# Kernel optimization log

Hardware: AMD Instinct MI355X
Metric: run time of the kernel (lower is better)

The kernel has to match this reference:

```python
import math
import jax, jax.numpy as jnp
import numpy as np
from jax import lax

# Block_mamba(dim=192): x = x + Mamba(LN1(x)); x = x + EinFFT(LN2(x), H, W)
DIM = 192
D_STATE = 64
D_CONV = 4
EXPAND = 2
D_INNER = EXPAND * DIM          # 384
DT_RANK = math.ceil(DIM / 16)   # 12
NUM_BLOCKS = 4                  # EinFFT hardcoded
BLOCK_SIZE = DIM // NUM_BLOCKS  # 48
LAMBDA = 0.01                   # softshrink threshold


def setup_inputs() -> dict:
    key = jax.random.key(0)
    ks = jax.random.split(key, 20)
    B, N, C = 4, 1024, DIM
    s = 0.02
    x = jax.random.normal(ks[0], (B, N, C), jnp.float32)
    inp = {
        "x": x,
        "ln1_w": jnp.ones((C,), jnp.float32),
        "ln1_b": jnp.zeros((C,), jnp.float32),
        "in_proj_w": jax.random.normal(ks[1], (2 * D_INNER, C), jnp.float32) * s,
        "conv_w": jax.random.normal(ks[2], (D_INNER, 1, D_CONV), jnp.float32) * 0.1,
        "conv_b": jnp.zeros((D_INNER,), jnp.float32),
        "x_proj_w": jax.random.normal(ks[3], (DT_RANK + 2 * D_STATE, D_INNER), jnp.float32) * s,
        "dt_proj_w": jax.random.normal(ks[4], (D_INNER, DT_RANK), jnp.float32) * (DT_RANK ** -0.5),
        "dt_proj_b": jax.random.uniform(ks[5], (D_INNER,), jnp.float32, -4.0, -2.0),
        "A_log": jnp.log(jnp.broadcast_to(jnp.arange(1, D_STATE + 1, dtype=jnp.float32), (D_INNER, D_STATE))),
        "D": jnp.ones((D_INNER,), jnp.float32),
        "out_proj_w": jax.random.normal(ks[6], (C, D_INNER), jnp.float32) * s,
        "ln2_w": jnp.ones((C,), jnp.float32),
        "ln2_b": jnp.zeros((C,), jnp.float32),
        "cw1": jax.random.normal(ks[7], (2, NUM_BLOCKS, BLOCK_SIZE, BLOCK_SIZE), jnp.float32) * s,
        "cw2": jax.random.normal(ks[8], (2, NUM_BLOCKS, BLOCK_SIZE, BLOCK_SIZE), jnp.float32) * s,
        "cb1": jax.random.normal(ks[9], (2, NUM_BLOCKS, BLOCK_SIZE), jnp.float32) * s,
        "cb2": jax.random.normal(ks[10], (2, NUM_BLOCKS, BLOCK_SIZE), jnp.float32) * s,
        "H": 32,
        "W": 32,
    }
    return inp


def layer_norm(x, w, b, eps=1e-5):
    mu = jnp.mean(x, axis=-1, keepdims=True)
    var = jnp.var(x, axis=-1, keepdims=True)
    return (x - mu) * lax.rsqrt(var + eps) * w + b


def mamba(x, in_proj_w, conv_w, conv_b, x_proj_w, dt_proj_w, dt_proj_b, A_log, D):
    B, L, C = x.shape
    xz = jnp.einsum('blc,ec->ble', x, in_proj_w)          # [B,L,2*D_INNER]
    xm, z = jnp.split(xz, 2, axis=-1)                      # each [B,L,D_INNER]
    # causal depthwise conv1d (torch pads both sides then slices [:, :, :L])
    xc = lax.conv_general_dilated(
        xm.transpose(0, 2, 1), conv_w, (1,), [(D_CONV - 1, 0)],
        dimension_numbers=('NCH', 'OIH', 'NCH'), feature_group_count=D_INNER)
    xm = jax.nn.silu(xc + conv_b[None, :, None]).transpose(0, 2, 1)  # [B,L,D_INNER]
    dbc = jnp.einsum('bld,ed->ble', xm, x_proj_w)
    dt, Bm, Cm = jnp.split(dbc, [DT_RANK, DT_RANK + D_STATE], axis=-1)
    delta = jax.nn.softplus(jnp.einsum('blr,dr->bld', dt, dt_proj_w) + dt_proj_b)  # [B,L,D_INNER]
    A = -jnp.exp(A_log)                                    # [D_INNER, D_STATE]

    def step(h, inp):
        d_t, B_t, C_t, x_t = inp                           # [B,d],[B,n],[B,n],[B,d]
        dA = jnp.exp(d_t[:, :, None] * A)                  # [B,d,n]
        h = h * dA + (d_t * x_t)[:, :, None] * B_t[:, None, :]
        y = jnp.einsum('bdn,bn->bd', h, C_t)
        return h, y

    h0 = jnp.zeros((B, D_INNER, D_STATE), x.dtype)
    xs = (delta.transpose(1, 0, 2), Bm.transpose(1, 0, 2), Cm.transpose(1, 0, 2), xm.transpose(1, 0, 2))
    _, ys = lax.scan(step, h0, xs)                         # ys: [L,B,d]
    y = ys.transpose(1, 0, 2) + xm * D
    y = y * jax.nn.silu(z)
    return jnp.einsum('bld,cd->blc', y, out_proj_w_global[0])


# small trick to keep mamba signature tidy
out_proj_w_global = [None]


def einfft(x, cw1, cw2, cb1, cb2):
    B, N, C = x.shape
    xv = x.reshape(B, N, NUM_BLOCKS, BLOCK_SIZE)
    pad1 = (1 << math.ceil(math.log2(N))) - N
    pad2 = (1 << math.ceil(math.log2(NUM_BLOCKS))) - NUM_BLOCKS
    if pad1 or pad2:
        xv = jnp.pad(xv, ((0, 0), (0, pad1), (0, pad2), (0, 0)))
    X = jnp.fft.fft2(xv, axes=(1, 2), norm='ortho')
    mul = lambda t, w: jnp.einsum('Bnbd,bdk->Bnbk', t, w)
    r1 = jax.nn.relu(mul(X.real, cw1[0]) - mul(X.imag, cw1[1]) + cb1[0])
    i1 = jax.nn.relu(mul(X.real, cw1[1]) + mul(X.imag, cw1[0]) + cb1[1])
    r2 = mul(r1, cw2[0]) - mul(i1, cw2[1]) + cb2[0]
    i2 = mul(r1, cw2[1]) + mul(i1, cw2[0]) + cb2[1]
    ss = lambda v: jnp.where(v > LAMBDA, v - LAMBDA, jnp.where(v < -LAMBDA, v + LAMBDA, jnp.zeros((), v.dtype)))
    Z = ss(r2) + 1j * ss(i2)
    y = jnp.fft.ifft2(Z, axes=(1, 2), norm='ortho')[:, :N, :NUM_BLOCKS, :]
    return y.real.reshape(B, N, C)  # torch .to(real dtype) keeps real part


def reference(x, ln1_w, ln1_b, in_proj_w, conv_w, conv_b, x_proj_w, dt_proj_w, dt_proj_b,
              A_log, D, out_proj_w, ln2_w, ln2_b, cw1, cw2, cb1, cb2, H, W):
    out_proj_w_global[0] = out_proj_w
    x = x + mamba(layer_norm(x, ln1_w, ln1_b), in_proj_w, conv_w, conv_b,
                  x_proj_w, dt_proj_w, dt_proj_b, A_log, D)
    x = x + einfft(layer_norm(x, ln2_w, ln2_b), cw1, cw2, cb1, cb2)
    return x
```

## Files before the change

kernel.cpp:

```cpp
#include <hip/hip_runtime.h>
#include <math.h>

#define PI_F 3.14159265358979323846f

__device__ __forceinline__ float lane_bcast(float v, int l) {
  return __int_as_float(__builtin_amdgcn_readlane(__float_as_int(v), l));
}

__device__ __forceinline__ float wave_reduce_sum(float v) {
  v += __shfl_xor(v, 32, 64);
  v += __shfl_xor(v, 16, 64);
  v += __shfl_xor(v, 8, 64);
  v += __shfl_xor(v, 4, 64);
  v += __shfl_xor(v, 2, 64);
  v += __shfl_xor(v, 1, 64);
  return v;
}

__global__ __launch_bounds__(256) void ln_kernel(const float* __restrict__ x,
    const float* __restrict__ w, const float* __restrict__ b, float* __restrict__ o) {
  int row = blockIdx.x * 4 + (threadIdx.x >> 6);
  int lane = threadIdx.x & 63;
  const float* xr = x + (size_t)row * 192;
  float v0 = xr[lane], v1 = xr[lane + 64], v2 = xr[lane + 128];
  float s  = wave_reduce_sum(v0 + v1 + v2);
  float s2 = wave_reduce_sum(v0 * v0 + v1 * v1 + v2 * v2);
  float mu  = s * (1.f / 192.f);
  float var = s2 * (1.f / 192.f) - mu * mu;
  float rs  = rsqrtf(var + 1e-5f);
  float* orow = o + (size_t)row * 192;
  orow[lane]       = (v0 - mu) * rs * w[lane]       + b[lane];
  orow[lane + 64]  = (v1 - mu) * rs * w[lane + 64]  + b[lane + 64];
  orow[lane + 128] = (v2 - mu) * rs * w[lane + 128] + b[lane + 128];
}

__global__ __launch_bounds__(256) void ln2t_kernel(const float* __restrict__ x,
    const float* __restrict__ w, const float* __restrict__ b, float* __restrict__ xT) {
  __shared__ float xt[32][193];
  __shared__ float mu_s[32], rs_s[32];
  int blk = blockIdx.x;
  int Bi = blk >> 5;
  int t0 = (blk & 31) * 32;
  int tid = threadIdx.x;
  const float* xb = x + ((size_t)(Bi * 1024 + t0)) * 192;
  for (int i = tid; i < 32 * 192; i += 256) {
    xt[i / 192][i % 192] = xb[i];
  }
  __syncthreads();
  int row = tid >> 3, seg = tid & 7;
  float s = 0.f, s2 = 0.f;
  const float* xr = &xt[row][seg * 24];
#pragma unroll
  for (int k = 0; k < 24; ++k) { float v = xr[k]; s += v; s2 += v * v; }
  s  += __shfl_xor(s, 1, 64);  s  += __shfl_xor(s, 2, 64);  s  += __shfl_xor(s, 4, 64);
  s2 += __shfl_xor(s2, 1, 64); s2 += __shfl_xor(s2, 2, 64); s2 += __shfl_xor(s2, 4, 64);
  if (seg == 0) {
    float mu = s * (1.f / 192.f);
    float var = s2 * (1.f / 192.f) - mu * mu;
    mu_s[row] = mu;
    rs_s[row] = rsqrtf(var + 1e-5f);
  }
  __syncthreads();
  for (int i = tid; i < 32 * 192; i += 256) {
    int ch = i >> 5, r2 = i & 31;
    float v = (xt[r2][ch] - mu_s[r2]) * rs_s[r2] * w[ch] + b[ch];
    xT[((size_t)(Bi * 192 + ch)) * 1024 + t0 + r2] = v;
  }
}

__global__ __launch_bounds__(256) void gemm_tn(const float* __restrict__ A,
    const float* __restrict__ W, const float* __restrict__ res, float* __restrict__ C,
    int M, int N, int K) {
  __shared__ float As[2][32][68];
  __shared__ float Ws[2][32][68];
  int tid = threadIdx.x;
  int m0 = blockIdx.y * 64, n0 = blockIdx.x * 64;
  int tr = tid >> 4, tc = tid & 15;
  int sm  = tid >> 3;
  int skq = tid & 7;
  float4 aP[2], wP[2];
#pragma unroll
  for (int j = 0; j < 2; ++j) {
    int m = sm + j * 32;
    aP[j] = *(const float4*)(A + (size_t)(m0 + m) * K + skq * 4);
    int n = n0 + m;
    if (n < N) wP[j] = *(const float4*)(W + (size_t)n * K + skq * 4);
    else       wP[j] = make_float4(0.f, 0.f, 0.f, 0.f);
  }
#pragma unroll
  for (int j = 0; j < 2; ++j) {
    int m = sm + j * 32;
    As[0][skq * 4 + 0][m] = aP[j].x;
    As[0][skq * 4 + 1][m] = aP[j].y;
    As[0][skq * 4 + 2][m] = aP[j].z;
    As[0][skq * 4 + 3][m] = aP[j].w;
    Ws[0][skq * 4 + 0][m] = wP[j].x;
    Ws[0][skq * 4 + 1][m] = wP[j].y;
    Ws[0][skq * 4 + 2][m] = wP[j].z;
    Ws[0][skq * 4 + 3][m] = wP[j].w;
  }
  __syncthreads();
  float acc[4][4] = {{0.f}};
  int nk = K >> 5;
  for (int it = 0; it < nk; ++it) {
    int cur = it & 1, nxt = cur ^ 1;
    if (it + 1 < nk) {
      int kk = (it + 1) << 5;
#pragma unroll
      for (int j = 0; j < 2; ++j) {
        int m = sm + j * 32;
        aP[j] = *(const float4*)(A + (size_t)(m0 + m) * K + kk + skq * 4);
        int n = n0 + m;
        if (n < N) wP[j] = *(const float4*)(W + (size_t)n * K + kk + skq * 4);
        else       wP[j] = make_float4(0.f, 0.f, 0.f, 0.f);
      }
    }
#pragma unroll
    for (int k = 0; k < 32; ++k) {
      float4 a4 = *(const float4*)&As[cur][k][tr * 4];
      float4 w4 = *(const float4*)&Ws[cur][k][tc * 4];
      float a[4] = {a4.x, a4.y, a4.z, a4.w};
      float bb[4] = {w4.x, w4.y, w4.z, w4.w};
#pragma unroll
      for (int i = 0; i < 4; ++i)
#pragma unroll
        for (int j = 0; j < 4; ++j)
          acc[i][j] = fmaf(a[i], bb[j], acc[i][j]);
    }
    if (it + 1 < nk) {
#pragma unroll
      for (int j = 0; j < 2; ++j) {
        int m = sm + j * 32;
        As[nxt][skq * 4 + 0][m] = aP[j].x;
        As[nxt][skq * 4 + 1][m] = aP[j].y;
        As[nxt][skq * 4 + 2][m] = aP[j].z;
        As[nxt][skq * 4 + 3][m] = aP[j].w;
        Ws[nxt][skq * 4 + 0][m] = wP[j].x;
        Ws[nxt][skq * 4 + 1][m] = wP[j].y;
        Ws[nxt][skq * 4 + 2][m] = wP[j].z;
        Ws[nxt][skq * 4 + 3][m] = wP[j].w;
      }
      __syncthreads();
    }
  }
#pragma unroll
  for (int i = 0; i < 4; ++i) {
    int m = m0 + tr * 4 + i;
#pragma unroll
    for (int j = 0; j < 4; ++j) {
      int n = n0 + tc * 4 + j;
      if (n < N) {
        float v = acc[i][j];
        if (res) v += res[m * N + n];
        C[m * N + n] = v;
      }
    }
  }
}

__global__ __launch_bounds__(256) void gemm_tn32(const float* __restrict__ A,
    const float* __restrict__ W, const float* __restrict__ res, float* __restrict__ C,
    int M, int N, int K) {
  __shared__ float As[2][32][36];
  __shared__ float Ws[2][32][68];
  int tid = threadIdx.x;
  int m0 = blockIdx.y * 32, n0 = blockIdx.x * 64;
  int tr = tid >> 4, tc = tid & 15;
  int sm  = tid >> 3;
  int skq = tid & 7;
  float4 aP, wP[2];
  aP = *(const float4*)(A + (size_t)(m0 + sm) * K + skq * 4);
#pragma unroll
  for (int j = 0; j < 2; ++j) {
    int n = n0 + sm + j * 32;
    if (n < N) wP[j] = *(const float4*)(W + (size_t)n * K + skq * 4);
    else       wP[j] = make_float4(0.f, 0.f, 0.f, 0.f);
  }
  As[0][skq * 4 + 0][sm] = aP.x;
  As[0][skq * 4 + 1][sm] = aP.y;
  As[0][skq * 4 + 2][sm] = aP.z;
  As[0][skq * 4 + 3][sm] = aP.w;
#pragma unroll
  for (int j = 0; j < 2; ++j) {
    int n = sm + j * 32;
    Ws[0][skq * 4 + 0][n] = wP[j].x;
    Ws[0][skq * 4 + 1][n] = wP[j].y;
    Ws[0][skq * 4 + 2][n] = wP[j].z;
    Ws[0][skq * 4 + 3][n] = wP[j].w;
  }
  __syncthreads();
  float acc[2][4] = {{0.f}};
  int nk = K >> 5;
  for (int it = 0; it < nk; ++it) {
    int cur = it & 1, nxt = cur ^ 1;
    if (it + 1 < nk) {
      int kk = (it + 1) << 5;
      aP = *(const float4*)(A + (size_t)(m0 + sm) * K + kk + skq * 4);
#pragma unroll
      for (int j = 0; j < 2; ++j) {
        int n = n0 + sm + j * 32;
        if (n < N) wP[j] = *(const float4*)(W + (size_t)n * K + kk + skq * 4);
        else       wP[j] = make_float4(0.f, 0.f, 0.f, 0.f);
      }
    }
#pragma unroll
    for (int k = 0; k < 32; ++k) {
      float2 a2 = *(const float2*)&As[cur][k][tr * 2];
      float4 w4 = *(const float4*)&Ws[cur][k][tc * 4];
      float a[2] = {a2.x, a2.y};
      float bb[4] = {w4.x, w4.y, w4.z, w4.w};
#pragma unroll
      for (int i = 0; i < 2; ++i)
#pragma unroll
        for (int j = 0; j < 4; ++j)
          acc[i][j] = fmaf(a[i], bb[j], acc[i][j]);
    }
    if (it + 1 < nk) {
      As[nxt][skq * 4 + 0][sm] = aP.x;
      As[nxt][skq * 4 + 1][sm] = aP.y;
      As[nxt][skq * 4 + 2][sm] = aP.z;
      As[nxt][skq * 4 + 3][sm] = aP.w;
#pragma unroll
      for (int j = 0; j < 2; ++j) {
        int n = sm + j * 32;
        Ws[nxt][skq * 4 + 0][n] = wP[j].x;
        Ws[nxt][skq * 4 + 1][n] = wP[j].y;
        Ws[nxt][skq * 4 + 2][n] = wP[j].z;
        Ws[nxt][skq * 4 + 3][n] = wP[j].w;
      }
      __syncthreads();
    }
  }
#pragma unroll
  for (int i = 0; i < 2; ++i) {
    int m = m0 + tr * 2 + i;
#pragma unroll
    for (int j = 0; j < 4; ++j) {
      int n = n0 + tc * 4 + j;
      if (n < N) {
        float v = acc[i][j];
        if (res) v += res[m * N + n];
        C[m * N + n] = v;
      }
    }
  }
}

__global__ __launch_bounds__(256) void gemm_at32(const float* __restrict__ AT,
    const float* __restrict__ W, const float* __restrict__ res, float* __restrict__ C,
    int M, int N, int K) {
  __shared__ float As[2][32][36];
  __shared__ float Ws[2][32][68];
  int tid = threadIdx.x;
  int m0 = blockIdx.y * 32, n0 = blockIdx.x * 64;
  int bb = m0 >> 10;
  int t0 = m0 & 1023;
  const float* Ab = AT + ((size_t)bb * K) * 1024 + t0;
  int tr = tid >> 4, tc = tid & 15;
  int sm  = tid >> 3;
  int skq = tid & 7;
  float4 aP, wP[2];
  aP = *(const float4*)(Ab + (size_t)sm * 1024 + skq * 4);
#pragma unroll
  for (int j = 0; j < 2; ++j) {
    int n = n0 + sm + j * 32;
    if (n < N) wP[j] = *(const float4*)(W + (size_t)n * K + skq * 4);
    else       wP[j] = make_float4(0.f, 0.f, 0.f, 0.f);
  }
  *(float4*)&As[0][sm][skq * 4] = aP;
#pragma unroll
  for (int j = 0; j < 2; ++j) {
    int n = sm + j * 32;
    Ws[0][skq * 4 + 0][n] = wP[j].x;
    Ws[0][skq * 4 + 1][n] = wP[j].y;
    Ws[0][skq * 4 + 2][n] = wP[j].z;
    Ws[0][skq * 4 + 3][n] = wP[j].w;
  }
  __syncthreads();
  float acc[2][4] = {{0.f}};
  int nk = K >> 5;
  for (int it = 0; it < nk; ++it) {
    int cur = it & 1, nxt = cur ^ 1;
    if (it + 1 < nk) {
      int kk = (it + 1) << 5;
      aP = *(const float4*)(Ab + (size_t)(kk + sm) * 1024 + skq * 4);
#pragma unroll
      for (int j = 0; j < 2; ++j) {
        int n = n0 + sm + j * 32;
        if (n < N) wP[j] = *(const float4*)(W + (size_t)n * K + kk + skq * 4);
        else       wP[j] = make_float4(0.f, 0.f, 0.f, 0.f);
      }
    }
#pragma unroll
    for (int k = 0; k < 32; ++k) {
      float2 a2 = *(const float2*)&As[cur][k][tr * 2];
      float4 w4 = *(const float4*)&Ws[cur][k][tc * 4];
      float a[2] = {a2.x, a2.y};
      float bb4[4] = {w4.x, w4.y, w4.z, w4.w};
#pragma unroll
      for (int i = 0; i < 2; ++i)
#pragma unroll
        for (int j = 0; j < 4; ++j)
          acc[i][j] = fmaf(a[i], bb4[j], acc[i][j]);
    }
    if (it + 1 < nk) {
      *(float4*)&As[nxt][sm][skq * 4] = aP;
#pragma unroll
      for (int j = 0; j < 2; ++j) {
        int n = sm + j * 32;
        Ws[nxt][skq * 4 + 0][n] = wP[j].x;
        Ws[nxt][skq * 4 + 1][n] = wP[j].y;
        Ws[nxt][skq * 4 + 2][n] = wP[j].z;
        Ws[nxt][skq * 4 + 3][n] = wP[j].w;
      }
      __syncthreads();
    }
  }
#pragma unroll
  for (int i = 0; i < 2; ++i) {
    int m = m0 + tr * 2 + i;
#pragma unroll
    for (int j = 0; j < 4; ++j) {
      int n = n0 + tc * 4 + j;
      if (n < N) {
        float v = acc[i][j];
        if (res) v += res[m * N + n];
        C[m * N + n] = v;
      }
    }
  }
}

__global__ __launch_bounds__(256) void conv_silu(const float* __restrict__ xz,
    const float* __restrict__ cw, const float* __restrict__ cb, float* __restrict__ xc) {
  int e4 = blockIdx.x * 256 + threadIdx.x;
  if (e4 >= 4 * 1024 * 96) return;
  int d4 = e4 % 96;
  int t  = (e4 / 96) % 1024;
  int b  = e4 / (96 * 1024);
  int d = d4 * 4;
  const float* base = xz + (size_t)(b * 1024) * 768 + d;
  float4 acc = *(const float4*)(cb + d);
  const float4* cwv = (const float4*)(cw + d * 4);
  float4 c0 = cwv[0], c1 = cwv[1], c2 = cwv[2], c3 = cwv[3];
#pragma unroll
  for (int j = 0; j < 4; ++j) {
    int tt = t - 3 + j;
    if (tt >= 0) {
      float4 v = *(const float4*)(base + (size_t)tt * 768);
      float w0 = (&c0.x)[j], w1 = (&c1.x)[j], w2 = (&c2.x)[j], w3 = (&c3.x)[j];
      acc.x = fmaf(v.x, w0, acc.x);
      acc.y = fmaf(v.y, w1, acc.y);
      acc.z = fmaf(v.z, w2, acc.z);
      acc.w = fmaf(v.w, w3, acc.w);
    }
  }
  float4 o;
  o.x = acc.x / (1.f + __expf(-acc.x));
  o.y = acc.y / (1.f + __expf(-acc.y));
  o.z = acc.z / (1.f + __expf(-acc.z));
  o.w = acc.w / (1.f + __expf(-acc.w));
  *(float4*)(xc + ((size_t)(b * 1024 + t) * 384) + d) = o;
}

__global__ __launch_bounds__(256) void delta_trans(const float* __restrict__ dbc,
    const float* __restrict__ dtw, const float* __restrict__ dtb,
    const float* __restrict__ xc, float* __restrict__ dltT, float* __restrict__ duT) {
  __shared__ float dts[64][13];
  __shared__ float xt[64][65];
  int blk = blockIdx.x;
  int b  = blk / 96;
  int rem = blk % 96;
  int tt = rem / 6, dd = rem % 6;
  int t0 = tt * 64, d0 = dd * 64;
  int tid = threadIdx.x;
  for (int i = tid; i < 64 * 12; i += 256) {
    int tl = i / 12, r = i % 12;
    dts[tl][r] = dbc[((size_t)b * 1024 + t0 + tl) * 140 + r];
  }
  {
    int col = tid & 63, rg = tid >> 6;
#pragma unroll
    for (int j = 0; j < 16; ++j) {
      int row = j * 4 + rg;
      xt[row][col] = xc[((size_t)b * 1024 + t0 + row) * 384 + d0 + col];
    }
  }
  __syncthreads();
  int tl = tid & 63, grp = tid >> 6;
#pragma unroll
  for (int j = 0; j < 16; ++j) {
    int dl = grp * 16 + j;
    int d = d0 + dl;
    float s = dtb[d];
#pragma unroll
    for (int r = 0; r < 12; ++r) s += dts[tl][r] * dtw[d * 12 + r];
    float dlt = (s > 20.f) ? s : log1pf(__expf(s));
    size_t ob = ((size_t)b * 384 + d) * 1024 + t0 + tl;
    dltT[ob] = dlt;
    duT[ob]  = dlt * xt[tl][dl];
  }
}

__global__ __launch_bounds__(512) void scan_fused(const float* __restrict__ dltT,
    const float* __restrict__ duT, const float* __restrict__ dbc,
    const float* __restrict__ A_log, const float* __restrict__ xc,
    const float* __restrict__ xz, const float* __restrict__ Dvec,
    float* __restrict__ yT) {
  __shared__ float tile[8][16][65];
  __shared__ float psP[8][64];
  __shared__ float psS[8][64];
  int bd = blockIdx.x;
  int b = bd / 384, d = bd % 384;
  int tid = threadIdx.x;
  int c = tid >> 6;
  int lane = tid & 63;
  float A = -__expf(A_log[d * 64 + lane]) * 1.44269504f;
  int t0 = c * 128;
  const float* dT = dltT + ((size_t)b * 384 + d) * 1024 + t0;
  const float* uT = duT  + ((size_t)b * 384 + d) * 1024 + t0;
  const float* Bp = dbc + ((size_t)b * 1024 + t0) * 140 + 12 + lane;
  const float* Cp = Bp + 64;
  float Pv = 1.f, Sv = 0.f;
#pragma unroll
  for (int half = 0; half < 2; ++half) {
    float dv64 = dT[half * 64 + lane];
    float du64 = uT[half * 64 + lane];
    for (int tb = 0; tb < 64; tb += 16) {
      float Bv[16];
#pragma unroll
      for (int i = 0; i < 16; ++i)
        Bv[i] = Bp[(size_t)(half * 64 + tb + i) * 140];
#pragma unroll
      for (int i = 0; i < 16; ++i) {
        float sdv = lane_bcast(dv64, tb + i);
        float sdu = lane_bcast(du64, tb + i);
        float a = exp2f(sdv * A);
        Pv *= a;
        Sv = fmaf(Sv, a, sdu * Bv[i]);
      }
    }
  }
  psP[c][lane] = Pv;
  psS[c][lane] = Sv;
  __syncthreads();
  float h = 0.f;
  for (int k = 0; k < c; ++k)
    h = fmaf(psP[k][lane], h, psS[k][lane]);
  float ddv = Dvec[d];
  float* yp = yT + ((size_t)b * 384 + d) * 1024 + t0;
  const float* xcp = xc + ((size_t)b * 1024 + t0) * 384 + d;
  const float* xzp = xz + ((size_t)b * 1024 + t0) * 768 + 384 + d;
  int tq = lane & 15;
  int q  = lane >> 4;
#pragma unroll
  for (int half = 0; half < 2; ++half) {
    float dv64 = dT[half * 64 + lane];
    float du64 = uT[half * 64 + lane];
    for (int tb = 0; tb < 64; tb += 16) {
      int ts = half * 64 + tb;
      float Bv[16], Cv[16];
#pragma unroll
      for (int i = 0; i < 16; ++i) {
        size_t ro = (size_t)(ts + i) * 140;
        Bv[i] = Bp[ro];
        Cv[i] = Cp[ro];
      }
      float xcv = 0.f, zv = 0.f;
      if (lane < 16) {
        xcv = xcp[(size_t)(ts + lane) * 384];
        zv  = xzp[(size_t)(ts + lane) * 768];
      }
#pragma unroll
      for (int i = 0; i < 16; ++i) {
        float sdv = lane_bcast(dv64, tb + i);
        float sdu = lane_bcast(du64, tb + i);
        float a = exp2f(sdv * A);
        h = fmaf(h, a, sdu * Bv[i]);
        tile[c][i][lane] = h * Cv[i];
      }
      const float* trow = &tile[c][tq][q * 16];
      float s = 0.f;
#pragma unroll
      for (int i = 0; i < 16; ++i) s += trow[i];
      s += __shfl_xor(s, 16, 64);
      s += __shfl_xor(s, 32, 64);
      if (lane < 16) {
        float sg = zv / (1.f + __expf(-zv));
        yp[ts + lane] = (s + xcv * ddv) * sg;
      }
    }
  }
}

__device__ __forceinline__ int rev4_10(int i) {
  unsigned r = __brev((unsigned)i) >> 22;
  return (int)(((r & 0x155u) << 1) | ((r >> 1) & 0x155u));
}

__device__ __forceinline__ void fft1024r4(float* __restrict__ re,
    float* __restrict__ im, const float* __restrict__ twc,
    const float* __restrict__ tws, int tid, float sgn) {
  for (int i = tid; i < 1024; i += 256) {
    int r = rev4_10(i);
    if (i < r) {
      float t = re[i]; re[i] = re[r]; re[r] = t;
      t = im[i]; im[i] = im[r]; im[r] = t;
    }
  }
  __syncthreads();
  {
    float4 ar = *(float4*)&re[tid * 4];
    float4 ai = *(float4*)&im[tid * 4];
    float apc_r = ar.x + ar.z, amc_r = ar.x - ar.z;
    float apc_i = ai.x + ai.z, amc_i = ai.x - ai.z;
    float bpd_r = ar.y + ar.w, bmd_r = ar.y - ar.w;
    float bpd_i = ai.y + ai.w, bmd_i = ai.y - ai.w;
    float4 yr, yi;
    yr.x = apc_r + bpd_r;        yi.x = apc_i + bpd_i;
    yr.z = apc_r - bpd_r;        yi.z = apc_i - bpd_i;
    yr.y = amc_r - sgn * bmd_i;  yi.y = amc_i + sgn * bmd_r;
    yr.w = amc_r + sgn * bmd_i;  yi.w = amc_i - sgn * bmd_r;
    *(float4*)&re[tid * 4] = yr;
    *(float4*)&im[tid * 4] = yi;
  }
  __syncthreads();
#pragma unroll
  for (int s = 1; s < 5; ++s) {
    int L = 1 << (2 * s);
    int tstep = 256 >> (2 * s);
    int j = tid & (L - 1);
    int base = ((tid >> (2 * s)) << (2 * s + 2)) + j;
    int i0 = base, i1 = base + L, i2 = base + 2 * L, i3 = base + 3 * L;
    int x1i = j * tstep;
    float w1c = twc[x1i],     w1s = tws[x1i];
    float w2c = twc[2 * x1i], w2s = tws[2 * x1i];
    float w3c = twc[3 * x1i], w3s = tws[3 * x1i];
    float ar_ = re[i0], ai_ = im[i0];
    float br_ = re[i1], bi_ = im[i1];
    float cr_ = re[i2], ci_ = im[i2];
    float dr_ = re[i3], di_ = im[i3];
    float tbr = br_ * w1c - bi_ * w1s, tbi = br_ * w1s + bi_ * w1c;
    float tcr = cr_ * w2c - ci_ * w2s, tci = cr_ * w2s + ci_ * w2c;
    float tdr = dr_ * w3c - di_ * w3s, tdi = dr_ * w3s + di_ * w3c;
    float apc_r = ar_ + tcr, amc_r = ar_ - tcr;
    float apc_i = ai_ + tci, amc_i = ai_ - tci;
    float bpd_r = tbr + tdr, bmd_r = tbr - tdr;
    float bpd_i = tbi + tdi, bmd_i = tbi - tdi;
    re[i0] = apc_r + bpd_r;       im[i0] = apc_i + bpd_i;
    re[i2] = apc_r - bpd_r;       im[i2] = apc_i - bpd_i;
    re[i1] = amc_r - sgn * bmd_i; im[i1] = amc_i + sgn * bmd_r;
    re[i3] = amc_r + sgn * bmd_i; im[i3] = amc_i - sgn * bmd_r;
    __syncthreads();
  }
}

__global__ __launch_bounds__(256) void fft_fwd(const float* __restrict__ x2T,
    float* __restrict__ Xre, float* __restrict__ Xim) {
  __shared__ float re[1024];
  __shared__ float im[1024];
  __shared__ float twc[768];
  __shared__ float tws[768];
  int blk = blockIdx.x;
  int c = blk & 3;
  int rest = blk >> 2;
  int d = rest % 48, Bi = rest / 48;
  int tid = threadIdx.x;
  for (int k = tid; k < 768; k += 256) {
    float sv, cv;
    __sincosf(-PI_F * (float)k * (1.f / 512.f), &sv, &cv);
    twc[k] = cv; tws[k] = sv;
  }
  const float* pb = x2T + ((size_t)(Bi * 192 + d)) * 1024;
  for (int n = tid; n < 1024; n += 256) {
    float v0 = pb[n];
    float v1 = pb[48 * 1024 + n];
    float v2 = pb[96 * 1024 + n];
    float v3 = pb[144 * 1024 + n];
    float rr, ii;
    if (c == 0)      { rr = v0 + v1 + v2 + v3; ii = 0.f; }
    else if (c == 1) { rr = v0 - v2;           ii = -(v1 - v3); }
    else if (c == 2) { rr = v0 - v1 + v2 - v3; ii = 0.f; }
    else             { rr = v0 - v2;           ii = (v1 - v3); }
    re[n] = rr; im[n] = ii;
  }
  __syncthreads();
  fft1024r4(re, im, twc, tws, tid, -1.0f);
  float* xo_r = Xre + ((size_t)((Bi * 4 + c) * 48 + d)) * 1024;
  float* xo_i = Xim + ((size_t)((Bi * 4 + c) * 48 + d)) * 1024;
  for (int k = tid; k < 1024; k += 256) {
    xo_r[k] = re[k] * (1.f / 64.f);
    xo_i[k] = im[k] * (1.f / 64.f);
  }
}

__global__ __launch_bounds__(256) void mix_fused(float* __restrict__ Xre,
    float* __restrict__ Xim, const float* __restrict__ cw1,
    const float* __restrict__ cw2, const float* __restrict__ cb1,
    const float* __restrict__ cb2) {
  __shared__ float r1s[4][48][4];
  __shared__ float i1s[4][48][4];
  int w = threadIdx.x >> 6;
  int j = threadIdx.x & 63;
  int rg = blockIdx.x * 4 + w;
  int kq = rg & 255;
  int b  = (rg >> 8) & 3;
  int Bi = rg >> 10;
  int k0 = kq * 4;
  size_t xbase = ((size_t)((Bi * 4 + b) * 48)) * 1024 + k0;
  if (j < 48) {
    const float* wr = cw1 + b * 2304;
    const float* wi = cw1 + 9216 + b * 2304;
    float b1r = cb1[b * 48 + j], b1i = cb1[192 + b * 48 + j];
    float ar[4] = {b1r, b1r, b1r, b1r};
    float ai[4] = {b1i, b1i, b1i, b1i};
#pragma unroll 8
    for (int dd = 0; dd < 48; ++dd) {
      float4 xr = *(const float4*)(Xre + xbase + (size_t)dd * 1024);
      float4 xi = *(const float4*)(Xim + xbase + (size_t)dd * 1024);
      float wrv = wr[dd * 48 + j], wiv = wi[dd * 48 + j];
      ar[0] = fmaf(xr.x, wrv, ar[0]); ar[0] = fmaf(-xi.x, wiv, ar[0]);
      ai[0] = fmaf(xr.x, wiv, ai[0]); ai[0] = fmaf(xi.x, wrv, ai[0]);
      ar[1] = fmaf(xr.y, wrv, ar[1]); ar[1] = fmaf(-xi.y, wiv, ar[1]);
      ai[1] = fmaf(xr.y, wiv, ai[1]); ai[1] = fmaf(xi.y, wrv, ai[1]);
      ar[2] = fmaf(xr.z, wrv, ar[2]); ar[2] = fmaf(-xi.z, wiv, ar[2]);
      ai[2] = fmaf(xr.z, wiv, ai[2]); ai[2] = fmaf(xi.z, wrv, ai[2]);
      ar[3] = fmaf(xr.w, wrv, ar[3]); ar[3] = fmaf(-xi.w, wiv, ar[3]);
      ai[3] = fmaf(xr.w, wiv, ai[3]); ai[3] = fmaf(xi.w, wrv, ai[3]);
    }
    float4 r1v, i1v;
    r1v.x = fmaxf(ar[0], 0.f); r1v.y = fmaxf(ar[1], 0.f);
    r1v.z = fmaxf(ar[2], 0.f); r1v.w = fmaxf(ar[3], 0.f);
    i1v.x = fmaxf(ai[0], 0.f); i1v.y = fmaxf(ai[1], 0.f);
    i1v.z = fmaxf(ai[2], 0.f); i1v.w = fmaxf(ai[3], 0.f);
    *(float4*)&r1s[w][j][0] = r1v;
    *(float4*)&i1s[w][j][0] = i1v;
    const float* wr2 = cw2 + b * 2304;
    const float* wi2 = cw2 + 9216 + b * 2304;
    float b2r = cb2[b * 48 + j], b2i = cb2[192 + b * 48 + j];
    float a2r[4] = {b2r, b2r, b2r, b2r};
    float a2i[4] = {b2i, b2i, b2i, b2i};
#pragma unroll 8
    for (int dd = 0; dd < 48; ++dd) {
      float4 rv = *(const float4*)&r1s[w][dd][0];
      float4 iv = *(const float4*)&i1s[w][dd][0];
      float wrv = wr2[dd * 48 + j], wiv = wi2[dd * 48 + j];
      a2r[0] = fmaf(rv.x, wrv, a2r[0]); a2r[0] = fmaf(-iv.x, wiv, a2r[0]);
      a2i[0] = fmaf(rv.x, wiv, a2i[0]); a2i[0] = fmaf(iv.x, wrv, a2i[0]);
      a2r[1] = fmaf(rv.y, wrv, a2r[1]); a2r[1] = fmaf(-iv.y, wiv, a2r[1]);
      a2i[1] = fmaf(rv.y, wiv, a2i[1]); a2i[1] = fmaf(iv.y, wrv, a2i[1]);
      a2r[2] = fmaf(rv.z, wrv, a2r[2]); a2r[2] = fmaf(-iv.z, wiv, a2r[2]);
      a2i[2] = fmaf(rv.z, wiv, a2i[2]); a2i[2] = fmaf(iv.z, wrv, a2i[2]);
      a2r[3] = fmaf(rv.w, wrv, a2r[3]); a2r[3] = fmaf(-iv.w, wiv, a2r[3]);
      a2i[3] = fmaf(rv.w, wiv, a2i[3]); a2i[3] = fmaf(iv.w, wrv, a2i[3]);
    }
    float4 zr, zi;
#pragma unroll
    for (int r = 0; r < 4; ++r) {
      float vr = a2r[r], vi = a2i[r];
      (&zr.x)[r] = (vr > 0.01f) ? vr - 0.01f : ((vr < -0.01f) ? vr + 0.01f : 0.f);
      (&zi.x)[r] = (vi > 0.01f) ? vi - 0.01f : ((vi < -0.01f) ? vi + 0.01f : 0.f);
    }
    size_t obase = ((size_t)((Bi * 4 + b) * 48 + j)) * 1024 + k0;
    *(float4*)(Xre + obase) = zr;
    *(float4*)(Xim + obase) = zi;
  }
}

__global__ __launch_bounds__(256) void fft_inv(const float* __restrict__ Zre,
    const float* __restrict__ Zim, const float* __restrict__ x1, float* __restrict__ out) {
  __shared__ float re[1024];
  __shared__ float im[1024];
  __shared__ float twc[768];
  __shared__ float tws[768];
  int blk = blockIdx.x;
  int c = blk & 3;
  int rest = blk >> 2;
  int d = rest % 48, Bi = rest / 48;
  int tid = threadIdx.x;
  for (int k = tid; k < 768; k += 256) {
    float sv, cv;
    __sincosf(PI_F * (float)k * (1.f / 512.f), &sv, &cv);
    twc[k] = cv; tws[k] = sv;
  }
  const float* zr0 = Zre + ((size_t)((Bi * 4) * 48 + d)) * 1024;
  const float* zi0 = Zim + ((size_t)((Bi * 4) * 48 + d)) * 1024;
  const int cs = 48 * 1024;
  for (int k = tid; k < 1024; k += 256) {
    float r0 = zr0[k], r1v = zr0[cs + k], r2 = zr0[2 * cs + k], r3 = zr0[3 * cs + k];
    float i0 = zi0[k], i1v = zi0[cs + k], i2 = zi0[2 * cs + k], i3 = zi0[3 * cs + k];
    float rr, ii;
    if (c == 0)      { rr = r0 + r1v + r2 + r3;  ii = i0 + i1v + i2 + i3; }
    else if (c == 1) { rr = r0 - i1v - r2 + i3;  ii = i0 + r1v - i2 - r3; }
    else if (c == 2) { rr = r0 - r1v + r2 - r3;  ii = i0 - i1v + i2 - i3; }
    else             { rr = r0 + i1v - r2 - i3;  ii = i0 - r1v - i2 + r3; }
    re[k] = rr; im[k] = ii;
  }
  __syncthreads();
  fft1024r4(re, im, twc, tws, tid, 1.0f);
  for (int n = tid; n < 1024; n += 256) {
    size_t o = (size_t)(Bi * 1024 + n) * 192 + c * 48 + d;
    out[o] = x1[o] + re[n] * (1.f / 64.f);
  }
}

extern "C" void kernel_launch(void* const* d_in, const int* in_sizes, int n_in,
                              void* d_out, int out_size, void* d_ws, size_t ws_size,
                              hipStream_t stream) {
  const float* x         = (const float*)d_in[0];
  const float* ln1_w     = (const float*)d_in[1];
  const float* ln1_b     = (const float*)d_in[2];
  const float* in_proj_w = (const float*)d_in[3];
  const float* conv_w    = (const float*)d_in[4];
  const float* conv_b    = (const float*)d_in[5];
  const float* x_proj_w  = (const float*)d_in[6];
  const float* dt_proj_w = (const float*)d_in[7];
  const float* dt_proj_b = (const float*)d_in[8];
  const float* A_log     = (const float*)d_in[9];
  const float* Dvec      = (const float*)d_in[10];
  const float* out_proj_w= (const float*)d_in[11];
  const float* ln2_w     = (const float*)d_in[12];
  const float* ln2_b     = (const float*)d_in[13];
  const float* cw1       = (const float*)d_in[14];
  const float* cw2       = (const float*)d_in[15];
  const float* cb1       = (const float*)d_in[16];
  const float* cb2       = (const float*)d_in[17];
  float* out = (float*)d_out;
  float* ws  = (float*)d_ws;

  float* xz   = ws;
  float* xc   = xz  + 3145728;
  float* dbc  = xc  + 1572864;
  float* dltT = dbc + 573440;
  float* yvT  = dltT + 1572864;
  float* xln  = yvT + 1572864;
  float* x2T  = xln + 786432;
  float* Xre  = x2T + 786432;
  float* Xim  = Xre + 786432;
  float* duT = Xre;
  float* x1 = xln;

  ln_kernel<<<1024, 256, 0, stream>>>(x, ln1_w, ln1_b, xln);
  gemm_tn<<<dim3(12, 64), 256, 0, stream>>>(xln, in_proj_w, nullptr, xz, 4096, 768, 192);
  conv_silu<<<1536, 256, 0, stream>>>(xz, conv_w, conv_b, xc);
  gemm_tn32<<<dim3(3, 128), 256, 0, stream>>>(xc, x_proj_w, nullptr, dbc, 4096, 140, 384);
  delta_trans<<<384, 256, 0, stream>>>(dbc, dt_proj_w, dt_proj_b, xc, dltT, duT);
  scan_fused<<<1536, 512, 0, stream>>>(dltT, duT, dbc, A_log, xc, xz, Dvec, yvT);
  gemm_at32<<<dim3(3, 128), 256, 0, stream>>>(yvT, out_proj_w, x, x1, 4096, 192, 384);
  ln2t_kernel<<<128, 256, 0, stream>>>(x1, ln2_w, ln2_b, x2T);
  fft_fwd<<<768, 256, 0, stream>>>(x2T, Xre, Xim);
  mix_fused<<<1024, 256, 0, stream>>>(Xre, Xim, cw1, cw2, cb1, cb2);
  fft_inv<<<768, 256, 0, stream>>>(Xre, Xim, x1, out);
}
```

Baseline: 340.2 us.

## Replace chunked parallel scan with single-wave sequential scan per channel

The selective scan previously split each (batch, channel) sequence into 8 chunks handled by 8 waves. It ran a first pass to build chunk prefix products and sums, combined them through shared memory, then ran a second pass. Now one 64-lane wave walks the full 1024 steps sequentially, removing the first pass, the barrier and the cross-chunk combine. The trade-off is a serial dependency chain 8x longer per block and only 1536 single-wave blocks to hide latency, which may leave the GPU underoccupied.

```diff
diff --git a/kernel.cpp b/kernel.cpp
--- a/kernel.cpp
+++ b/kernel.cpp
@@ -402,63 +402,32 @@
   }
 }
 
-__global__ __launch_bounds__(512) void scan_fused(const float* __restrict__ dltT,
+__global__ __launch_bounds__(64) void scan_single(const float* __restrict__ dltT,
     const float* __restrict__ duT, const float* __restrict__ dbc,
     const float* __restrict__ A_log, const float* __restrict__ xc,
     const float* __restrict__ xz, const float* __restrict__ Dvec,
     float* __restrict__ yT) {
-  __shared__ float tile[8][16][65];
-  __shared__ float psP[8][64];
-  __shared__ float psS[8][64];
+  __shared__ float tile[16][65];
   int bd = blockIdx.x;
   int b = bd / 384, d = bd % 384;
-  int tid = threadIdx.x;
-  int c = tid >> 6;
-  int lane = tid & 63;
+  int lane = threadIdx.x;
   float A = -__expf(A_log[d * 64 + lane]) * 1.44269504f;
-  int t0 = c * 128;
-  const float* dT = dltT + ((size_t)b * 384 + d) * 1024 + t0;
-  const float* uT = duT  + ((size_t)b * 384 + d) * 1024 + t0;
-  const float* Bp = dbc + ((size_t)b * 1024 + t0) * 140 + 12 + lane;
+  const float* dT = dltT + ((size_t)b * 384 + d) * 1024;
+  const float* uT = duT  + ((size_t)b * 384 + d) * 1024;
+  const float* Bp = dbc + ((size_t)b * 1024) * 140 + 12 + lane;
   const float* Cp = Bp + 64;
-  float Pv = 1.f, Sv = 0.f;
-#pragma unroll
-  for (int half = 0; half < 2; ++half) {
-    float dv64 = dT[half * 64 + lane];
-    float du64 = uT[half * 64 + lane];
-    for (int tb = 0; tb < 64; tb += 16) {
-      float Bv[16];
-#pragma unroll
-      for (int i = 0; i < 16; ++i)
-        Bv[i] = Bp[(size_t)(half * 64 + tb + i) * 140];
-#pragma unroll
-      for (int i = 0; i < 16; ++i) {
-        float sdv = lane_bcast(dv64, tb + i);
-        float sdu = lane_bcast(du64, tb + i);
-        float a = exp2f(sdv * A);
-        Pv *= a;
-        Sv = fmaf(Sv, a, sdu * Bv[i]);
-      }
-    }
-  }
-  psP[c][lane] = Pv;
-  psS[c][lane] = Sv;
-  __syncthreads();
-  float h = 0.f;
-  for (int k = 0; k < c; ++k)
-    h = fmaf(psP[k][lane], h, psS[k][lane]);
   float ddv = Dvec[d];
-  float* yp = yT + ((size_t)b * 384 + d) * 1024 + t0;
-  const float* xcp = xc + ((size_t)b * 1024 + t0) * 384 + d;
-  const float* xzp = xz + ((size_t)b * 1024 + t0) * 768 + 384 + d;
+  float* yp = yT + ((size_t)b * 384 + d) * 1024;
+  const float* xcp = xc + ((size_t)b * 1024) * 384 + d;
+  const float* xzp = xz + ((size_t)b * 1024) * 768 + 384 + d;
   int tq = lane & 15;
   int q  = lane >> 4;
-#pragma unroll
-  for (int half = 0; half < 2; ++half) {
-    float dv64 = dT[half * 64 + lane];
-    float du64 = uT[half * 64 + lane];
+  float h = 0.f;
+  for (int seg = 0; seg < 16; ++seg) {
+    float dv64 = dT[seg * 64 + lane];
+    float du64 = uT[seg * 64 + lane];
     for (int tb = 0; tb < 64; tb += 16) {
-      int ts = half * 64 + tb;
+      int ts = seg * 64 + tb;
       float Bv[16], Cv[16];
 #pragma unroll
       for (int i = 0; i < 16; ++i) {
@@ -477,9 +446,9 @@
         float sdu = lane_bcast(du64, tb + i);
         float a = exp2f(sdv * A);
         h = fmaf(h, a, sdu * Bv[i]);
-        tile[c][i][lane] = h * Cv[i];
-      }
-      const float* trow = &tile[c][tq][q * 16];
+        tile[i][lane] = h * Cv[i];
+      }
+      const float* trow = &tile[tq][q * 16];
       float s = 0.f;
 #pragma unroll
       for (int i = 0; i < 16; ++i) s += trow[i];
@@ -745,7 +714,7 @@
   conv_silu<<<1536, 256, 0, stream>>>(xz, conv_w, conv_b, xc);
   gemm_tn32<<<dim3(3, 128), 256, 0, stream>>>(xc, x_proj_w, nullptr, dbc, 4096, 140, 384);
   delta_trans<<<384, 256, 0, stream>>>(dbc, dt_proj_w, dt_proj_b, xc, dltT, duT);
-  scan_fused<<<1536, 512, 0, stream>>>(dltT, duT, dbc, A_log, xc, xz, Dvec, yvT);
+  scan_single<<<1536, 64, 0, stream>>>(dltT, duT, dbc, A_log, xc, xz, Dvec, yvT);
   gemm_at32<<<dim3(3, 128), 256, 0, stream>>>(yvT, out_proj_w, x, x1, 4096, 192, 384);
   ln2t_kernel<<<128, 256, 0, stream>>>(x1, ln2_w, ln2_b, x2T);
   fft_fwd<<<768, 256, 0, stream>>>(x2T, Xre, Xim);
```

New measurement: 342.4 us. About the same (+0.7%).
